# Kernel optimization log

Hardware: AMD Instinct MI355X
Metric: run time of the kernel (lower is better)

Reference implementation:

```python
import jax, jax.numpy as jnp
import numpy as np
import math

B, N, D, H, K, HID, FF = 4, 4096, 256, 4, 16, 64, 1024
DH = D // H
EPS = 1e-5


def setup_inputs() -> dict:
    key = jax.random.key(0)
    ks = jax.random.split(key, 24)
    s = 0.02
    inp = {
        'xyz': jax.random.uniform(ks[0], (B, N, 3), dtype=jnp.float32),
        'feats': jax.random.normal(ks[1], (B, N, D), dtype=jnp.float32),
        'ln_q_g': jnp.ones((D,), jnp.float32),
        'ln_q_b': jnp.zeros((D,), jnp.float32),
        'Wq': jax.random.normal(ks[2], (D, D), jnp.float32) * s,
        'bq': jnp.zeros((D,), jnp.float32),
        'Wk': jax.random.normal(ks[3], (D, D), jnp.float32) * s,
        'bk': jnp.zeros((D,), jnp.float32),
        'Wv': jax.random.normal(ks[4], (D, D), jnp.float32) * s,
        'bv': jnp.zeros((D,), jnp.float32),
        'W_rel1': jax.random.normal(ks[5], (4, HID), jnp.float32) * s,
        'b_rel1': jnp.zeros((HID,), jnp.float32),
        'W_rel2': jax.random.normal(ks[6], (HID, D), jnp.float32) * s,
        'b_rel2': jnp.zeros((D,), jnp.float32),
        'Wo': jax.random.normal(ks[7], (D, D), jnp.float32) * s,
        'bo': jnp.zeros((D,), jnp.float32),
        'ln_f_g': jnp.ones((D,), jnp.float32),
        'ln_f_b': jnp.zeros((D,), jnp.float32),
        'W_ff1': jax.random.normal(ks[8], (D, FF), jnp.float32) * s,
        'b_ff1': jnp.zeros((FF,), jnp.float32),
        'W_ff2': jax.random.normal(ks[9], (FF, D), jnp.float32) * s,
        'b_ff2': jnp.zeros((D,), jnp.float32),
    }
    return inp


def _layernorm(x, g, b):
    mu = jnp.mean(x, axis=-1, keepdims=True)
    var = jnp.var(x, axis=-1, keepdims=True)
    return (x - mu) * jax.lax.rsqrt(var + EPS) * g + b


def _knn_indices(xyz, k):
    # pairwise squared distances (B, N, N); exclude self via +inf diagonal
    sq = jnp.sum(xyz * xyz, axis=-1)  # (B, N)
    d2 = sq[:, :, None] + sq[:, None, :] - 2.0 * jnp.einsum('bnc,bmc->bnm', xyz, xyz)
    d2 = d2 + jnp.eye(xyz.shape[1], dtype=xyz.dtype) * 1e9
    _, idx = jax.lax.top_k(-d2, k)  # (B, N, k) nearest neighbors
    return idx


def _index_points(pts, idx):
    # pts: (B, N, C), idx: (B, N, k) -> (B, N, k, C)
    return jax.vmap(lambda p, i: p[i])(pts, idx)


def reference(xyz, feats, ln_q_g, ln_q_b, Wq, bq, Wk, bk, Wv, bv,
              W_rel1, b_rel1, W_rel2, b_rel2, Wo, bo,
              ln_f_g, ln_f_b, W_ff1, b_ff1, W_ff2, b_ff2):
    k = min(K, N - 1)
    idx = _knn_indices(xyz, k)

    x = _layernorm(feats, ln_q_g, ln_q_b)
    q = x @ Wq + bq
    k_lin = x @ Wk + bk
    v_lin = x @ Wv + bv

    k_nb = _index_points(k_lin, idx)   # (B,N,k,D)
    v_nb = _index_points(v_lin, idx)   # (B,N,k,D)
    nb_xyz = _index_points(xyz, idx)   # (B,N,k,3)

    diff = nb_xyz - xyz[:, :, None, :]
    rel = jnp.concatenate([diff, jnp.linalg.norm(diff, axis=-1, keepdims=True)], axis=-1)  # (B,N,k,4)
    rel_e = jax.nn.gelu(rel @ W_rel1 + b_rel1, approximate=False) @ W_rel2 + b_rel2

    k_nb = k_nb + rel_e
    v_nb = v_nb + rel_e

    qh = q.reshape(B, N, H, DH)              # (B,N,H,dh)
    kh = k_nb.reshape(B, N, k, H, DH)        # (B,N,k,H,dh)
    vh = v_nb.reshape(B, N, k, H, DH)

    attn = jnp.einsum('bnhc,bnkhc->bnhk', qh, kh) / math.sqrt(DH)
    attn = jax.nn.softmax(attn, axis=-1)
    out = jnp.einsum('bnhk,bnkhc->bnhc', attn, vh).reshape(B, N, D)
    out = out @ Wo + bo

    feats = feats + out
    h = _layernorm(feats, ln_f_g, ln_f_b)
    h = jax.nn.gelu(h @ W_ff1 + b_ff1, approximate=False) @ W_ff2 + b_ff2
    return feats + h
```

## Files before the change

### kernel.cpp

```cpp
#include <hip/hip_runtime.h>
#include <hip/hip_bf16.h>
#include <math.h>

#define NB 4
#define NPTS 4096
#define DIM 256
#define KNN 16
#define HID 64
#define FFDIM 1024
#define LN_EPS 1e-5f
#define MTOT (NB * NPTS)
#define KINF 3e38f
#define QPB 8

typedef __attribute__((ext_vector_type(8))) short short8;
typedef __attribute__((ext_vector_type(4))) float f32x4;

__device__ __forceinline__ float gelu_f(float x) {
    return 0.5f * x * (1.0f + erff(x * 0.7071067811865476f));
}
__device__ __forceinline__ float b2f(ushort u) {
    return __uint_as_float(((unsigned)u) << 16);
}
__device__ __forceinline__ ushort f2b(float f) {
    unsigned u = __float_as_uint(f);
    return (ushort)((u + 0x7fffu + ((u >> 16) & 1u)) >> 16);
}
__device__ __forceinline__ void gload16(const void* g, void* l) {
    __builtin_amdgcn_global_load_lds((const __attribute__((address_space(1))) void*)g,
                                     (__attribute__((address_space(3))) void*)l, 16, 0, 0);
}
__device__ __forceinline__ float dot8(uint4 w, const float* q) {
    float s = 0.f;
    s += b2f((ushort)(w.x & 0xffff)) * q[0]; s += b2f((ushort)(w.x >> 16)) * q[1];
    s += b2f((ushort)(w.y & 0xffff)) * q[2]; s += b2f((ushort)(w.y >> 16)) * q[3];
    s += b2f((ushort)(w.z & 0xffff)) * q[4]; s += b2f((ushort)(w.z >> 16)) * q[5];
    s += b2f((ushort)(w.w & 0xffff)) * q[6]; s += b2f((ushort)(w.w >> 16)) * q[7];
    return s;
}

__global__ __launch_bounds__(256) void knn_kernel(const float* __restrict__ xyz,
                                                  int* __restrict__ idx_out) {
    int blk = blockIdx.x;
    int bq0 = blk * QPB;
    int b = bq0 >> 12;
    const float* base = xyz + (size_t)b * NPTS * 3;
    int t = threadIdx.x;
    int lane = t & 63, wv = t >> 6;

    __shared__ float pxS[NPTS];
    __shared__ float pyS[NPTS];
    __shared__ float pzS[NPTS];
    __shared__ int   cnt[QPB];
    __shared__ float cV[QPB][64];
    __shared__ int   cI[QPB][64];

    if (t < QPB) cnt[t] = 0;
    for (int i = t; i < NPTS; i += 256) {
        pxS[i] = base[i * 3 + 0];
        pyS[i] = base[i * 3 + 1];
        pzS[i] = base[i * 3 + 2];
    }
    __syncthreads();

    #pragma unroll 1
    for (int rep = 0; rep < 2; ++rep) {
        int qi = wv + 4 * rep;
        int bn = bq0 + qi;
        int n = bn & (NPTS - 1);
        float qx = pxS[n], qy = pyS[n], qz = pzS[n];
        float sqn = qx * qx + qy * qy + qz * qz;

        float d[64];
        float lm = KINF;
        #pragma unroll
        for (int i = 0; i < 64; ++i) {
            int m = lane + 64 * i;
            float x = pxS[m], y = pyS[m], z = pzS[m];
            float sqm = x * x + y * y + z * z;
            float dot = qx * x + qy * y + qz * z;
            float dd = (sqn + sqm) - 2.0f * dot;
            d[i] = (m == n) ? KINF : dd;
            lm = fminf(lm, d[i]);
        }

        float v = lm;
        #pragma unroll
        for (int k = 2; k <= 64; k <<= 1) {
            #pragma unroll
            for (int j = 32; j > 0; j >>= 1) {
                if (j < k) {
                    float ov = __shfl_xor(v, j, 64);
                    bool keepMin = ((lane & k) == 0) == ((lane & j) == 0);
                    if (keepMin == (ov < v)) v = ov;
                }
            }
        }
        float T = __shfl(v, 15, 64);

        #pragma unroll
        for (int i = 0; i < 64; ++i) {
            if (d[i] <= T) {
                int pos = atomicAdd(&cnt[qi], 1);
                if (pos < 64) { cV[qi][pos] = d[i]; cI[qi][pos] = lane + 64 * i; }
            }
        }

        int nc = cnt[qi]; nc = nc > 64 ? 64 : nc;
        float v2 = (lane < nc) ? cV[qi][lane] : KINF;
        int   m2 = (lane < nc) ? cI[qi][lane] : 0x7fffffff;
        #pragma unroll
        for (int k = 2; k <= 64; k <<= 1) {
            #pragma unroll
            for (int j = 32; j > 0; j >>= 1) {
                if (j < k) {
                    float ov = __shfl_xor(v2, j, 64);
                    int   om = __shfl_xor(m2, j, 64);
                    bool keepMin = ((lane & k) == 0) == ((lane & j) == 0);
                    bool less = (ov < v2) || (ov == v2 && om < m2);
                    if (keepMin == less) { v2 = ov; m2 = om; }
                }
            }
        }
        if (lane < KNN) idx_out[(size_t)bn * KNN + lane] = m2;
    }
}

__global__ __launch_bounds__(256) void ln_kernel(const float* __restrict__ in,
                                                 const float* __restrict__ g,
                                                 const float* __restrict__ bb,
                                                 ushort* __restrict__ out) {
    int r = blockIdx.x;
    int t = threadIdx.x;
    float v = in[(size_t)r * DIM + t];

    __shared__ float sw[4];
    __shared__ float sw2[4];

    float s = v;
    #pragma unroll
    for (int off = 32; off > 0; off >>= 1) s += __shfl_down(s, off);
    if ((t & 63) == 0) sw[t >> 6] = s;
    __syncthreads();
    float mean = (sw[0] + sw[1] + sw[2] + sw[3]) * (1.0f / DIM);

    float dlt = v - mean;
    float s2 = dlt * dlt;
    #pragma unroll
    for (int off = 32; off > 0; off >>= 1) s2 += __shfl_down(s2, off);
    if ((t & 63) == 0) sw2[t >> 6] = s2;
    __syncthreads();
    float var = (sw2[0] + sw2[1] + sw2[2] + sw2[3]) * (1.0f / DIM);

    out[(size_t)r * DIM + t] = f2b(dlt * rsqrtf(var + LN_EPS) * g[t] + bb[t]);
}

__global__ __launch_bounds__(256) void tconv4(const float* __restrict__ s0,
                                              const float* __restrict__ s1,
                                              const float* __restrict__ s2,
                                              const float* __restrict__ s3,
                                              ushort* __restrict__ d0,
                                              ushort* __restrict__ d1,
                                              ushort* __restrict__ d2,
                                              ushort* __restrict__ d3) {
    const float* in; ushort* out;
    switch (blockIdx.z) {
        case 0: in = s0; out = d0; break;
        case 1: in = s1; out = d1; break;
        case 2: in = s2; out = d2; break;
        default: in = s3; out = d3; break;
    }
    __shared__ float tile[32][33];
    int tx = threadIdx.x & 31, ty = threadIdx.x >> 5;
    int r0 = blockIdx.y * 32, c0 = blockIdx.x * 32;
    #pragma unroll
    for (int k = 0; k < 4; ++k)
        tile[ty + 8 * k][tx] = in[(size_t)(r0 + ty + 8 * k) * 256 + c0 + tx];
    __syncthreads();
    #pragma unroll
    for (int k = 0; k < 4; ++k)
        out[(size_t)(c0 + ty + 8 * k) * 256 + r0 + tx] = f2b(tile[tx][ty + 8 * k]);
}

__global__ __launch_bounds__(256) void tconv(const float* __restrict__ in,
                                             ushort* __restrict__ out, int R, int C) {
    __shared__ float tile[32][33];
    int tx = threadIdx.x & 31, ty = threadIdx.x >> 5;
    int r0 = blockIdx.y * 32, c0 = blockIdx.x * 32;
    #pragma unroll
    for (int k = 0; k < 4; ++k)
        tile[ty + 8 * k][tx] = in[(size_t)(r0 + ty + 8 * k) * C + c0 + tx];
    __syncthreads();
    #pragma unroll
    for (int k = 0; k < 4; ++k)
        out[(size_t)(c0 + ty + 8 * k) * R + r0 + tx] = f2b(tile[tx][ty + 8 * k]);
}

__global__ __launch_bounds__(256) void prep_mats(const float* __restrict__ W2,
                                                 const float* __restrict__ Wq,
                                                 const ushort* __restrict__ WoT,
                                                 ushort* __restrict__ w2bd,
                                                 ushort* __restrict__ Wq_bf,
                                                 ushort* __restrict__ BtCat) {
    int bb = blockIdx.x, t = threadIdx.x;
    if (bb < 256) {
        float v = ((t >> 6) == (bb >> 6)) ? W2[(bb & 63) * 256 + t] : 0.0f;
        w2bd[bb * 256 + t] = f2b(v);
    } else if (bb < 512) {
        int r = bb - 256;
        Wq_bf[r * 256 + t] = f2b(Wq[r * 256 + t]);
    } else {
        int r = bb - 512;
        BtCat[(size_t)r * 512 + t] = WoT[r * 256 + t];
    }
}

__global__ __launch_bounds__(256) void prep_bias(const float* __restrict__ bq,
                                                 const float* __restrict__ bk,
                                                 const float* __restrict__ bv,
                                                 const float* __restrict__ W2,
                                                 const float* __restrict__ bo,
                                                 const float* __restrict__ br2,
                                                 const float* __restrict__ Wo,
                                                 float* __restrict__ bqkvw,
                                                 float* __restrict__ boc) {
    int bb = blockIdx.x, t = threadIdx.x;
    if (bb == 0) bqkvw[t] = bq[t];
    else if (bb == 1) bqkvw[256 + t] = bk[t];
    else if (bb == 2) bqkvw[512 + t] = bv[t];
    else if (bb == 3) {
        int h = t >> 6, i = t & 63;
        float s = 0.f;
        #pragma unroll 8
        for (int dp = 0; dp < 64; ++dp) s += bq[h * 64 + dp] * W2[i * 256 + h * 64 + dp];
        bqkvw[768 + t] = s;
    } else {
        float s = bo[t];
        #pragma unroll 8
        for (int d = 0; d < 256; ++d) s += br2[d] * Wo[d * 256 + t];
        boc[t] = s;
    }
}

template <int ACT, int OUTBF, int RES>
__global__ __launch_bounds__(256) void gemm_bt(
    const ushort* __restrict__ A, const ushort* __restrict__ Bt,
    const float* __restrict__ bias, const float* __restrict__ res,
    void* __restrict__ Cv, int M, int N, int K, int ldc)
{
    __shared__ ushort As[4096];
    __shared__ ushort Bs[4096];
    const int t = threadIdx.x;
    const int wave = t >> 6, lane = t & 63;
    const int m0 = blockIdx.y * 128, n0 = blockIdx.x * 128;
    const int wr = (wave >> 1) * 64, wc = (wave & 1) * 64;

    f32x4 acc[4][4];
    #pragma unroll
    for (int i = 0; i < 4; ++i)
        #pragma unroll
        for (int j = 0; j < 4; ++j) acc[i][j] = {0.f, 0.f, 0.f, 0.f};

    const int rA0 = (wave * 2 + 0) * 16 + (lane >> 2);
    const int rA1 = (wave * 2 + 1) * 16 + (lane >> 2);
    const int u4 = lane & 3;
    const int sw0 = (rA0 + (rA0 >> 2)) & 3;
    const int sw1 = (rA1 + (rA1 >> 2)) & 3;
    char* ldsA0 = (char*)As + (wave * 2 + 0) * 1024 + lane * 16;
    char* ldsA1 = (char*)As + (wave * 2 + 1) * 1024 + lane * 16;
    char* ldsB0 = (char*)Bs + (wave * 2 + 0) * 1024 + lane * 16;
    char* ldsB1 = (char*)Bs + (wave * 2 + 1) * 1024 + lane * 16;
    const size_t aOff0 = (size_t)(m0 + rA0) * K + (size_t)((u4 ^ sw0) * 8);
    const size_t aOff1 = (size_t)(m0 + rA1) * K + (size_t)((u4 ^ sw1) * 8);
    const size_t bOff0 = (size_t)(n0 + rA0) * K + (size_t)((u4 ^ sw0) * 8);
    const size_t bOff1 = (size_t)(n0 + rA1) * K + (size_t)((u4 ^ sw1) * 8);

    const int cl = lane & 15, gq = lane >> 4;

    for (int k0 = 0; k0 < K; k0 += 32) {
        gload16(A + aOff0 + k0, ldsA0);
        gload16(A + aOff1 + k0, ldsA1);
        gload16(Bt + bOff0 + k0, ldsB0);
        gload16(Bt + bOff1 + k0, ldsB1);
        __syncthreads();

        short8 av[4], bv[4];
        #pragma unroll
        for (int mi = 0; mi < 4; ++mi) {
            int row = wr + mi * 16 + cl;
            int s = (row + (row >> 2)) & 3;
            av[mi] = *(const short8*)((const char*)As + row * 64 + ((gq ^ s) << 4));
            int rowb = wc + mi * 16 + cl;
            int sb = (rowb + (rowb >> 2)) & 3;
            bv[mi] = *(const short8*)((const char*)Bs + rowb * 64 + ((gq ^ sb) << 4));
        }
        #pragma unroll
        for (int mi = 0; mi < 4; ++mi)
            #pragma unroll
            for (int ni = 0; ni < 4; ++ni)
                acc[mi][ni] = __builtin_amdgcn_mfma_f32_16x16x32_bf16(av[mi], bv[ni], acc[mi][ni], 0, 0, 0);
        __syncthreads();
    }

    float* Cf = (float*)Cv;
    ushort* Cb = (ushort*)Cv;
    #pragma unroll
    for (int ni = 0; ni < 4; ++ni) {
        int col = n0 + wc + ni * 16 + cl;
        float bvv = bias ? bias[col] : 0.0f;
        #pragma unroll
        for (int mi = 0; mi < 4; ++mi) {
            #pragma unroll
            for (int r = 0; r < 4; ++r) {
                int row = m0 + wr + mi * 16 + gq * 4 + r;
                float v = acc[mi][ni][r] + bvv;
                if (ACT == 1) v = gelu_f(v);
                if (RES) v += res[(size_t)row * N + col];
                if (OUTBF) Cb[(size_t)row * ldc + col] = f2b(v);
                else       Cf[(size_t)row * ldc + col] = v;
            }
        }
    }
}

#define PTS 8
__global__ __launch_bounds__(256) void attn_kernel(
    const int* __restrict__ idx,
    const ushort* __restrict__ qkvw,
    const float* __restrict__ xyz,
    const float* __restrict__ W1,
    const float* __restrict__ b1,
    ushort* __restrict__ ab)
{
    __shared__ float qS[256];
    __shared__ float qwS[256];
    __shared__ float psS[64];
    __shared__ uint4 hidS4[16 * 9];
    __shared__ int   nbAll[128];
    __shared__ float w1S[256];
    __shared__ float b1S[64];
    ushort* hidS = (ushort*)hidS4;

    const int t = threadIdx.x;
    const int h = t >> 6, lane = t & 63;
    const int bid = blockIdx.x;
    const int blk = ((bid & 7) << 8) | (bid >> 3);
    const int bn0 = blk * PTS;
    const int R0 = blk * (PTS * 16);

    if (t < 128) nbAll[t] = idx[R0 + t];
    w1S[t] = W1[t];
    if (t < 64) b1S[t] = b1[t];
    const float* xb3 = xyz + (size_t)(bn0 >> 12) * NPTS * 3;
    __syncthreads();

    for (int pt = 0; pt < PTS; ++pt) {
        const int bn = bn0 + pt;
        const size_t base = (size_t)(bn >> 12) * NPTS;

        qS[t]  = b2f(qkvw[(size_t)bn * 1024 + t]);
        qwS[t] = b2f(qkvw[(size_t)bn * 1024 + 768 + t]);
        {
            int n = bn & (NPTS - 1);
            float nx = xb3[n * 3 + 0], ny = xb3[n * 3 + 1], nz = xb3[n * 3 + 2];
            int j = t >> 4;
            int i0 = (t & 15) * 4;
            int m = nbAll[pt * 16 + j];
            float dx = xb3[m * 3 + 0] - nx;
            float dy = xb3[m * 3 + 1] - ny;
            float dz = xb3[m * 3 + 2] - nz;
            float nr = sqrtf(dx * dx + dy * dy + dz * dz);
            uint2 hw;
            float a0 = b1S[i0 + 0] + dx * w1S[i0 + 0] + dy * w1S[64 + i0 + 0] + dz * w1S[128 + i0 + 0] + nr * w1S[192 + i0 + 0];
            float a1 = b1S[i0 + 1] + dx * w1S[i0 + 1] + dy * w1S[64 + i0 + 1] + dz * w1S[128 + i0 + 1] + nr * w1S[192 + i0 + 1];
            float a2 = b1S[i0 + 2] + dx * w1S[i0 + 2] + dy * w1S[64 + i0 + 2] + dz * w1S[128 + i0 + 2] + nr * w1S[192 + i0 + 2];
            float a3 = b1S[i0 + 3] + dx * w1S[i0 + 3] + dy * w1S[64 + i0 + 3] + dz * w1S[128 + i0 + 3] + nr * w1S[192 + i0 + 3];
            hw.x = (uint)f2b(gelu_f(a0)) | ((uint)f2b(gelu_f(a1)) << 16);
            hw.y = (uint)f2b(gelu_f(a2)) | ((uint)f2b(gelu_f(a3)) << 16);
            *(uint2*)(hidS + j * 72 + i0) = hw;
        }
        __syncthreads();

        {
            int j = lane >> 2, sub = lane & 3;
            int m = nbAll[pt * 16 + j];
            const ushort* krow = qkvw + (base + m) * 1024 + 256 + h * 64 + sub * 16;
            uint4 ka = *(const uint4*)krow;
            uint4 kc = *(const uint4*)(krow + 8);
            const float* qp = &qS[h * 64 + sub * 16];
            float d1 = dot8(ka, qp) + dot8(kc, qp + 8);
            const ushort* hrow = hidS + j * 72 + sub * 16;
            uint4 ha = *(const uint4*)hrow;
            uint4 hc = *(const uint4*)(hrow + 8);
            const float* qwp = &qwS[h * 64 + sub * 16];
            float d2 = dot8(ha, qwp) + dot8(hc, qwp + 8);
            float pp = d1 + d2;
            pp += __shfl_xor(pp, 1, 64);
            pp += __shfl_xor(pp, 2, 64);
            pp *= 0.125f;
            float mx = pp;
            mx = fmaxf(mx, __shfl_xor(mx, 4, 64));
            mx = fmaxf(mx, __shfl_xor(mx, 8, 64));
            mx = fmaxf(mx, __shfl_xor(mx, 16, 64));
            mx = fmaxf(mx, __shfl_xor(mx, 32, 64));
            float e = expf(pp - mx);
            float ss = e;
            ss += __shfl_xor(ss, 4, 64);
            ss += __shfl_xor(ss, 8, 64);
            ss += __shfl_xor(ss, 16, 64);
            ss += __shfl_xor(ss, 32, 64);
            float pj = e / ss;
            if (sub == 0) psS[h * 16 + j] = pj;
        }
        __syncthreads();

        {
            float o = 0.f, hpv = 0.f;
            #pragma unroll
            for (int j = 0; j < 16; ++j) {
                float p = psS[h * 16 + j];
                int m = nbAll[pt * 16 + j];
                o   += p * b2f(qkvw[(base + m) * 1024 + 512 + t]);
                hpv += p * b2f(hidS[j * 72 + lane]);
            }
            ab[(size_t)bn * 512 + t]       = f2b(o);
            ab[(size_t)bn * 512 + 256 + t] = f2b(hpv);
        }
        __syncthreads();
    }
}

extern "C" void kernel_launch(void* const* d_in, const int* in_sizes, int n_in,
                              void* d_out, int out_size, void* d_ws, size_t ws_size,
                              hipStream_t stream) {
    const float* xyz    = (const float*)d_in[0];
    const float* feats  = (const float*)d_in[1];
    const float* ln_q_g = (const float*)d_in[2];
    const float* ln_q_b = (const float*)d_in[3];
    const float* Wq     = (const float*)d_in[4];
    const float* bq     = (const float*)d_in[5];
    const float* Wk     = (const float*)d_in[6];
    const float* bk     = (const float*)d_in[7];
    const float* Wv     = (const float*)d_in[8];
    const float* bv     = (const float*)d_in[9];
    const float* W_rel1 = (const float*)d_in[10];
    const float* b_rel1 = (const float*)d_in[11];
    const float* W_rel2 = (const float*)d_in[12];
    const float* b_rel2 = (const float*)d_in[13];
    const float* Wo     = (const float*)d_in[14];
    const float* bo     = (const float*)d_in[15];
    const float* ln_f_g = (const float*)d_in[16];
    const float* ln_f_b = (const float*)d_in[17];
    const float* W_ff1  = (const float*)d_in[18];
    const float* b_ff1  = (const float*)d_in[19];
    const float* W_ff2  = (const float*)d_in[20];
    const float* b_ff2  = (const float*)d_in[21];
    (void)in_sizes; (void)n_in; (void)out_size; (void)ws_size;

    char* ws = (char*)d_ws;
    const size_t MB = 1u << 20;
    int*    idx    = (int*)ws;
    ushort* xb     = (ushort*)(ws + 1 * MB);
    ushort* qkvw   = (ushort*)(ws + 9 * MB);
    ushort* ff1b   = (ushort*)(ws + 41 * MB);
    ushort* ab     = (ushort*)(ws + 73 * MB);
    ushort* BtQKVW = (ushort*)(ws + 89 * MB);
    ushort* WoT    = BtQKVW + 262144;
    ushort* Wf1T   = WoT + 65536;
    ushort* Wf2T   = Wf1T + 262144;
    ushort* Wq_bf  = Wf2T + 262144;
    ushort* w2bd   = Wq_bf + 65536;
    ushort* BtCat  = w2bd + 65536;
    float*  bqkvw  = (float*)(BtCat + 131072);
    float*  boc    = bqkvw + 1024;
    float*  feats1 = (float*)(ws + 9 * MB);
    ushort* hb     = xb;

    tconv4<<<dim3(8, 8, 4), 256, 0, stream>>>(Wq, Wk, Wv, Wo,
                                              BtQKVW, BtQKVW + 65536, BtQKVW + 131072, WoT);
    tconv<<<dim3(32, 8), 256, 0, stream>>>(W_ff1, Wf1T, 256, 1024);
    tconv<<<dim3(8, 32), 256, 0, stream>>>(W_ff2, Wf2T, 1024, 256);
    prep_mats<<<768, 256, 0, stream>>>(W_rel2, Wq, WoT, w2bd, Wq_bf, BtCat);
    gemm_bt<0, 1, 0><<<dim3(2, 2), 256, 0, stream>>>(w2bd, Wq_bf, nullptr, nullptr,
                                                     BtQKVW + 768 * 256, 256, 256, 256, 256);
    gemm_bt<0, 1, 0><<<dim3(2, 2), 256, 0, stream>>>(WoT, w2bd, nullptr, nullptr,
                                                     BtCat + 256, 256, 256, 256, 512);
    prep_bias<<<5, 256, 0, stream>>>(bq, bk, bv, W_rel2, bo, b_rel2, Wo, bqkvw, boc);

    knn_kernel<<<MTOT / QPB, 256, 0, stream>>>(xyz, idx);
    ln_kernel<<<MTOT, 256, 0, stream>>>(feats, ln_q_g, ln_q_b, xb);

    gemm_bt<0, 1, 0><<<dim3(8, 128), 256, 0, stream>>>(xb, BtQKVW, bqkvw, nullptr,
                                                       qkvw, MTOT, 1024, 256, 1024);

    attn_kernel<<<MTOT / PTS, 256, 0, stream>>>(idx, qkvw, xyz, W_rel1, b_rel1, ab);

    gemm_bt<0, 0, 1><<<dim3(2, 128), 256, 0, stream>>>(ab, BtCat, boc, feats, feats1, MTOT, 256, 512, 256);
    ln_kernel<<<MTOT, 256, 0, stream>>>(feats1, ln_f_g, ln_f_b, hb);
    gemm_bt<1, 1, 0><<<dim3(8, 128), 256, 0, stream>>>(hb, Wf1T, b_ff1, nullptr, ff1b, MTOT, 1024, 256, 1024);
    gemm_bt<0, 0, 1><<<dim3(2, 128), 256, 0, stream>>>(ff1b, Wf2T, b_ff2, feats1, (float*)d_out, MTOT, 256, 1024, 256);
}
```

Measured before the change: 283.7 us.

## Fuse KNN search and QKV projection GEMM into one heterogeneous launch

Merges the KNN kernel and the QKV(W) GEMM into a single launch of 3072 blocks, where every third block runs a 128x128 GEMM tile and the rest run KNN queries, sharing one static shared-memory buffer. The goal is to overlap the compute-bound GEMM with the latency- and shuffle-heavy KNN search on the same CUs and to drop one kernel launch. LN must now finish before KNN begins. The union shared memory of about 52KB is sized for KNN, which may limit occupancy for the GEMM blocks, and the inlined GEMM body may not match the tuning of the templated gemm_bt.

```diff
diff --git a/kernel.cpp b/kernel.cpp
--- a/kernel.cpp
+++ b/kernel.cpp
@@ -39,21 +39,21 @@
     return s;
 }
 
-__global__ __launch_bounds__(256) void knn_kernel(const float* __restrict__ xyz,
-                                                  int* __restrict__ idx_out) {
-    int blk = blockIdx.x;
+__device__ __forceinline__ void knn_body(char* smem, int blk,
+                                         const float* __restrict__ xyz,
+                                         int* __restrict__ idx_out) {
+    float* pxS = (float*)smem;
+    float* pyS = (float*)(smem + 16384);
+    float* pzS = (float*)(smem + 32768);
+    int*   cnt = (int*)(smem + 49152);
+    float (*cV)[64] = (float(*)[64])(smem + 49184);
+    int   (*cI)[64] = (int(*)[64])(smem + 51232);
+
     int bq0 = blk * QPB;
     int b = bq0 >> 12;
     const float* base = xyz + (size_t)b * NPTS * 3;
     int t = threadIdx.x;
     int lane = t & 63, wv = t >> 6;
-
-    __shared__ float pxS[NPTS];
-    __shared__ float pyS[NPTS];
-    __shared__ float pzS[NPTS];
-    __shared__ int   cnt[QPB];
-    __shared__ float cV[QPB][64];
-    __shared__ int   cI[QPB][64];
 
     if (t < QPB) cnt[t] = 0;
     for (int i = t; i < NPTS; i += 256) {
@@ -123,6 +123,96 @@
             }
         }
         if (lane < KNN) idx_out[(size_t)bn * KNN + lane] = m2;
+    }
+}
+
+__device__ __forceinline__ void gemm_body(char* smem, int bx, int by,
+                                          const ushort* __restrict__ A,
+                                          const ushort* __restrict__ Bt,
+                                          const float* __restrict__ bias,
+                                          ushort* __restrict__ Cb,
+                                          int N, int K, int ldc) {
+    ushort* As = (ushort*)smem;
+    ushort* Bs = (ushort*)(smem + 8192);
+    const int t = threadIdx.x;
+    const int wave = t >> 6, lane = t & 63;
+    const int m0 = by * 128, n0 = bx * 128;
+    const int wr = (wave >> 1) * 64, wc = (wave & 1) * 64;
+
+    f32x4 acc[4][4];
+    #pragma unroll
+    for (int i = 0; i < 4; ++i)
+        #pragma unroll
+        for (int j = 0; j < 4; ++j) acc[i][j] = {0.f, 0.f, 0.f, 0.f};
+
+    const int rA0 = (wave * 2 + 0) * 16 + (lane >> 2);
+    const int rA1 = (wave * 2 + 1) * 16 + (lane >> 2);
+    const int u4 = lane & 3;
+    const int sw0 = (rA0 + (rA0 >> 2)) & 3;
+    const int sw1 = (rA1 + (rA1 >> 2)) & 3;
+    char* ldsA0 = (char*)As + (wave * 2 + 0) * 1024 + lane * 16;
+    char* ldsA1 = (char*)As + (wave * 2 + 1) * 1024 + lane * 16;
+    char* ldsB0 = (char*)Bs + (wave * 2 + 0) * 1024 + lane * 16;
+    char* ldsB1 = (char*)Bs + (wave * 2 + 1) * 1024 + lane * 16;
+    const size_t aOff0 = (size_t)(m0 + rA0) * K + (size_t)((u4 ^ sw0) * 8);
+    const size_t aOff1 = (size_t)(m0 + rA1) * K + (size_t)((u4 ^ sw1) * 8);
+    const size_t bOff0 = (size_t)(n0 + rA0) * K + (size_t)((u4 ^ sw0) * 8);
+    const size_t bOff1 = (size_t)(n0 + rA1) * K + (size_t)((u4 ^ sw1) * 8);
+
+    const int cl = lane & 15, gq = lane >> 4;
+
+    for (int k0 = 0; k0 < K; k0 += 32) {
+        gload16(A + aOff0 + k0, ldsA0);
+        gload16(A + aOff1 + k0, ldsA1);
+        gload16(Bt + bOff0 + k0, ldsB0);
+        gload16(Bt + bOff1 + k0, ldsB1);
+        __syncthreads();
+
+        short8 av[4], bv[4];
+        #pragma unroll
+        for (int mi = 0; mi < 4; ++mi) {
+            int row = wr + mi * 16 + cl;
+            int s = (row + (row >> 2)) & 3;
+            av[mi] = *(const short8*)((const char*)As + row * 64 + ((gq ^ s) << 4));
+            int rowb = wc + mi * 16 + cl;
+            int sb = (rowb + (rowb >> 2)) & 3;
+            bv[mi] = *(const short8*)((const char*)Bs + rowb * 64 + ((gq ^ sb) << 4));
+        }
+        #pragma unroll
+        for (int mi = 0; mi < 4; ++mi)
+            #pragma unroll
+            for (int ni = 0; ni < 4; ++ni)
+                acc[mi][ni] = __builtin_amdgcn_mfma_f32_16x16x32_bf16(av[mi], bv[ni], acc[mi][ni], 0, 0, 0);
+        __syncthreads();
+    }
+
+    #pragma unroll
+    for (int ni = 0; ni < 4; ++ni) {
+        int col = n0 + wc + ni * 16 + cl;
+        float bvv = bias[col];
+        #pragma unroll
+        for (int mi = 0; mi < 4; ++mi) {
+            #pragma unroll
+            for (int r = 0; r < 4; ++r) {
+                int row = m0 + wr + mi * 16 + gq * 4 + r;
+                Cb[(size_t)row * ldc + col] = f2b(acc[mi][ni][r] + bvv);
+            }
+        }
+    }
+}
+
+__global__ __launch_bounds__(256) void knn_qkvw_kernel(
+    const float* __restrict__ xyz, int* __restrict__ idx_out,
+    const ushort* __restrict__ xb, const ushort* __restrict__ BtQKVW,
+    const float* __restrict__ bqkvw, ushort* __restrict__ qkvw)
+{
+    __shared__ char smem[53280];
+    int bid = blockIdx.x;
+    int g = bid / 3;
+    if (bid - g * 3 == 2) {
+        gemm_body(smem, g & 7, g >> 3, xb, BtQKVW, bqkvw, qkvw, 1024, 256, 1024);
+    } else {
+        knn_body(smem, bid - g, xyz, idx_out);
     }
 }
 
@@ -487,11 +577,9 @@
                                                      BtCat + 256, 256, 256, 256, 512);
     prep_bias<<<5, 256, 0, stream>>>(bq, bk, bv, W_rel2, bo, b_rel2, Wo, bqkvw, boc);
 
-    knn_kernel<<<MTOT / QPB, 256, 0, stream>>>(xyz, idx);
     ln_kernel<<<MTOT, 256, 0, stream>>>(feats, ln_q_g, ln_q_b, xb);
 
-    gemm_bt<0, 1, 0><<<dim3(8, 128), 256, 0, stream>>>(xb, BtQKVW, bqkvw, nullptr,
-                                                       qkvw, MTOT, 1024, 256, 1024);
+    knn_qkvw_kernel<<<3072, 256, 0, stream>>>(xyz, idx, xb, BtQKVW, bqkvw, qkvw);
 
     attn_kernel<<<MTOT / PTS, 256, 0, stream>>>(idx, qkvw, xyz, W_rel1, b_rel1, ab);
 
```

Result: slower. 346.4 us (+22.1%).
